# Kernel optimization log

Measured on AMD Instinct MI355X. Metric: run time of the kernel, lower is better.

The kernel has to match this reference:

```python
import jax, jax.numpy as jnp
import numpy as np

B, L, C = 32, 2048, 32
PL, STRIDE = 16, 16
P = L // PL
D, H_ENC, H_DEC, K, NH = 64, 256, 256, 512, 4
BETA, EPS, Q_EPS, CW = 0.25, 1e-5, 1e-5, 0.2


def setup_inputs() -> dict:
    key = jax.random.key(0)
    ks = jax.random.split(key, 16)
    g = lambda k, sh: 0.02 * jax.random.normal(k, sh, dtype=jnp.float32)
    return {
        'x': jax.random.normal(ks[0], (B, L, C), dtype=jnp.float32),
        'revin_w': jnp.ones((C,), jnp.float32), 'revin_b': jnp.zeros((C,), jnp.float32),
        'inp_W': g(ks[1], (PL, D)), 'inp_b': jnp.zeros((D,), jnp.float32),
        'Wq': g(ks[2], (D, D)), 'bq': jnp.zeros((D,), jnp.float32),
        'Wk': g(ks[3], (D, D)), 'bk': jnp.zeros((D,), jnp.float32),
        'Wv': g(ks[4], (D, D)), 'bv': jnp.zeros((D,), jnp.float32),
        'Wo': g(ks[5], (D, D)), 'bo': jnp.zeros((D,), jnp.float32),
        'ln1_g': jnp.ones((D,), jnp.float32), 'ln1_b': jnp.zeros((D,), jnp.float32),
        'ffn_W1': g(ks[6], (D, H_ENC)), 'ffn_b1': jnp.zeros((H_ENC,), jnp.float32),
        'ffn_W2': g(ks[7], (H_ENC, D)), 'ffn_b2': jnp.zeros((D,), jnp.float32),
        'ln2_g': jnp.ones((D,), jnp.float32), 'ln2_b': jnp.zeros((D,), jnp.float32),
        'codebook': jax.random.uniform(ks[8], (K, D), jnp.float32, -1.0 / K, 1.0 / K),
        'dec_W1': g(ks[9], (D, H_DEC)), 'dec_b1': jnp.zeros((H_DEC,), jnp.float32),
        'dec_W2': g(ks[10], (H_DEC, PL)), 'dec_b2': jnp.zeros((PL,), jnp.float32),
        'dec_Wr': g(ks[11], (D, PL)), 'dec_br': jnp.zeros((PL,), jnp.float32),
        'dec_ln_g': jnp.ones((PL,), jnp.float32), 'dec_ln_b': jnp.zeros((PL,), jnp.float32),
    }


def _layernorm(x, g, b):
    m = jnp.mean(x, -1, keepdims=True)
    v = jnp.mean((x - m) ** 2, -1, keepdims=True)
    return (x - m) * jax.lax.rsqrt(v + EPS) * g + b


def reference(x, revin_w, revin_b, inp_W, inp_b, Wq, bq, Wk, bk, Wv, bv, Wo, bo,
              ln1_g, ln1_b, ffn_W1, ffn_b1, ffn_W2, ffn_b2, ln2_g, ln2_b, codebook,
              dec_W1, dec_b1, dec_W2, dec_b2, dec_Wr, dec_br, dec_ln_g, dec_ln_b):
    # --- RevIN norm (stats over time dim) ---
    mean = jnp.mean(x, axis=1, keepdims=True)              # [B,1,C]
    std = jnp.sqrt(jnp.var(x, axis=1, keepdims=True) + EPS)
    xn = (x - mean) / std * revin_w + revin_b
    # --- patchify: [B,C,L] -> [B*C, P, PL] ---
    patches = jnp.transpose(xn, (0, 2, 1)).reshape(B * C, P, PL)
    # --- MHEncoder ---
    h = patches @ inp_W + inp_b                            # [N,P,D]
    dh = D // NH
    q = (h @ Wq + bq).reshape(-1, P, NH, dh)
    k = (h @ Wk + bk).reshape(-1, P, NH, dh)
    v = (h @ Wv + bv).reshape(-1, P, NH, dh)
    scores = jnp.einsum('nqhd,nkhd->nhqk', q, k) / np.sqrt(dh).astype(np.float32)
    attn = jax.nn.softmax(scores, axis=-1)
    a = jnp.einsum('nhqk,nkhd->nqhd', attn, v).reshape(-1, P, D)
    a = a @ Wo + bo
    h = _layernorm(h + a, ln1_g, ln1_b)
    ff = jax.nn.relu(h @ ffn_W1 + ffn_b1) @ ffn_W2 + ffn_b2
    h = _layernorm(h + ff, ln2_g, ln2_b)
    z = h.reshape(B, C, P, D)
    # --- ClusterQuantizer ---
    z2 = jnp.sum(z * z, -1, keepdims=True)                 # [B,V,P,1]
    e2 = jnp.sum(codebook * codebook, -1)                  # [K]
    ze = jnp.einsum('bvpd,kd->bvpk', z, codebook)
    dist = z2 + e2 - 2.0 * ze                              # [B,V,P,K]
    indices = jnp.argmin(dist, axis=-1)                    # [B,V,P] int
    z_q = codebook[indices]
    z_q_st = z + jax.lax.stop_gradient(z_q - z)
    codebook_loss = jnp.mean((z_q - jax.lax.stop_gradient(z)) ** 2)
    commitment_loss = jnp.mean((z - jax.lax.stop_gradient(z_q)) ** 2)
    cluster_loss = codebook_loss + BETA * commitment_loss
    counts = jnp.zeros((K,), jnp.float32).at[indices.ravel()].add(1.0)
    probs = counts / (counts.sum() + EPS)
    perplexity = jnp.exp(-jnp.sum(probs * jnp.log(probs + EPS)))
    # --- FFN decoder ---
    y = jax.nn.relu(z_q_st @ dec_W1 + dec_b1) @ dec_W2 + dec_b2
    y = y + z_q_st @ dec_Wr + dec_br
    recon_patches = _layernorm(y, dec_ln_g, dec_ln_b)      # [B,V,P,PL]
    recon = jnp.transpose(recon_patches.reshape(B, C, L), (0, 2, 1))  # [B,L,C]
    # --- RevIN denorm ---
    r = (recon - revin_b) / (revin_w + EPS * EPS) * std + mean
    rec_loss = jnp.mean((x - r) ** 2)
    loss_total = rec_loss + CW * cluster_loss
    return (loss_total, rec_loss, z_q_st, r, indices, perplexity)
```

## Files before the change

kernel.cpp:

```cpp
#include <hip/hip_runtime.h>
#include <math.h>

#define TPB 256

#define B_  32
#define L_  2048
#define C_  32
#define PL_ 16
#define P_  128
#define D_  64
#define HE_ 256
#define HD_ 256
#define K_  512
#define N_  1024
#define M_  131072

#define EPS_  1e-5f
#define BETA_ 0.25f
#define CW_   0.2f

#define OUT_LOSS 0
#define OUT_REC  1
#define OUT_ZQ   2
#define OUT_R    8388610
#define OUT_IDX  10485762
#define OUT_PERP 10616834

#define WS_MEAN   0
#define WS_STD    1024
#define WS_QT     2048
#define WS_KT     6144
#define WS_VT     10240
#define WS_E2     34816
#define WS_COUNTS 35328
#define WS_CPART  35840
#define WS_H0     36864
#define WS_H1     8425472
#define WS_RPART  WS_H1

__global__ void k_prep(const float* __restrict__ Wq, const float* __restrict__ Wk,
                       const float* __restrict__ Wv,
                       const float* __restrict__ cb, float* __restrict__ ws) {
    int g = blockIdx.x * TPB + threadIdx.x;
    if (g < 4096) { int t = g >> 6, j = g & 63; ws[WS_QT + g] = Wq[j * D_ + t]; }
    else if (g < 8192) { int g2 = g - 4096; int t = g2 >> 6, j = g2 & 63; ws[WS_KT + g2] = Wk[j * D_ + t]; }
    else if (g < 12288) { int g2 = g - 8192; int t = g2 >> 6, j = g2 & 63; ws[WS_VT + g2] = Wv[j * D_ + t]; }
    if (g < K_) {
        float s = 0.f;
        for (int j = 0; j < D_; j++) { float v = cb[g * D_ + j]; s += v * v; }
        ws[WS_E2 + g] = s;
    }
}

__global__ void k_stats(const float* __restrict__ x, float* __restrict__ ws) {
    int bc = blockIdx.x;
    int b = bc >> 5, c = bc & 31;
    const float* xp = x + (size_t)b * L_ * C_ + c;
    float s = 0.f, s2 = 0.f;
    for (int l = threadIdx.x; l < L_; l += TPB) { float v = xp[(size_t)l * C_]; s += v; s2 += v * v; }
    __shared__ float sh[TPB], sh2[TPB];
    sh[threadIdx.x] = s; sh2[threadIdx.x] = s2; __syncthreads();
    for (int o2 = 128; o2 > 0; o2 >>= 1) {
        if (threadIdx.x < o2) { sh[threadIdx.x] += sh[threadIdx.x + o2]; sh2[threadIdx.x] += sh2[threadIdx.x + o2]; }
        __syncthreads();
    }
    if (threadIdx.x == 0) {
        float m = sh[0] / (float)L_;
        float var = sh2[0] / (float)L_ - m * m;
        ws[WS_MEAN + bc] = m;
        ws[WS_STD + bc] = sqrtf(var + EPS_);
    }
}

__global__ __launch_bounds__(TPB) void k_embed(
    const float* __restrict__ x, const float* __restrict__ rw, const float* __restrict__ rb,
    const float* __restrict__ inpW, const float* __restrict__ inpb, float* __restrict__ ws) {
    int idx = blockIdx.x * TPB + threadIdx.x;
    int row = idx >> 6, d = idx & 63;
    int n = row >> 7, p = row & 127;
    int b = n >> 5, c = n & 31;
    float m = ws[WS_MEAN + n], sd = ws[WS_STD + n];
    float w = rw[c], bb = rb[c];
    const float* xp = x + (size_t)b * L_ * C_ + (size_t)p * PL_ * C_ + c;
    float acc = inpb[d];
#pragma unroll
    for (int j = 0; j < PL_; j++) {
        float xv = xp[(size_t)j * C_];
        float xn = (xv - m) / sd * w + bb;
        acc += xn * inpW[j * D_ + d];
    }
    ws[WS_H0 + (size_t)idx] = acc;
}

#define HSS  68
#define HS_  0
#define KH_  8704
#define VH_  10752
#define SMF  12800

__global__ __launch_bounds__(TPB) void k_attn(
    float* __restrict__ ws,
    const float* __restrict__ bq, const float* __restrict__ bk, const float* __restrict__ bv) {
    __shared__ float sm[SMF];
    const int tid = threadIdx.x;
    const int n = blockIdx.x >> 2, hh = blockIdx.x & 3;
    const float* h0 = ws + WS_H0 + (size_t)n * (P_ * D_);
    float* agl = ws + WS_H1 + (size_t)n * (P_ * D_);

    {
        const float4* h04 = (const float4*)h0;
#pragma unroll
        for (int it = 0; it < 8; ++it) {
            int e = tid + it * 256;
            int r = e >> 4, j4 = e & 15;
            *(float4*)(sm + HS_ + r * HSS + j4 * 4) = h04[e];
        }
    }
    __syncthreads();

    const int t_ = tid & 15, ib = tid >> 4;
    const float4* WqT4 = (const float4*)(ws + WS_QT);
    const float4* WkT4 = (const float4*)(ws + WS_KT);
    const float4* WvT4 = (const float4*)(ws + WS_VT);

    {
        float4 wreg[16];
        const float4* kr = WkT4 + (size_t)(hh * 16 + t_) * 16;
#pragma unroll
        for (int j4 = 0; j4 < 16; j4++) wreg[j4] = kr[j4];
        float bb = bk[hh * 16 + t_];
#pragma unroll
        for (int it = 0; it < 8; it++) {
            int i2 = ib + it * 16;
            const float4* hr = (const float4*)(sm + HS_ + i2 * HSS);
            float acc = bb;
#pragma unroll
            for (int j4 = 0; j4 < 16; j4++) {
                float4 h4 = hr[j4], w4 = wreg[j4];
                acc += h4.x * w4.x + h4.y * w4.y + h4.z * w4.z + h4.w * w4.w;
            }
            sm[KH_ + i2 * 16 + t_] = acc;
        }
    }
    {
        float4 wreg[16];
        const float4* vr = WvT4 + (size_t)(hh * 16 + t_) * 16;
#pragma unroll
        for (int j4 = 0; j4 < 16; j4++) wreg[j4] = vr[j4];
        float bb = bv[hh * 16 + t_];
#pragma unroll
        for (int it = 0; it < 8; it++) {
            int i2 = ib + it * 16;
            const float4* hr = (const float4*)(sm + HS_ + i2 * HSS);
            float acc = bb;
#pragma unroll
            for (int j4 = 0; j4 < 16; j4++) {
                float4 h4 = hr[j4], w4 = wreg[j4];
                acc += h4.x * w4.x + h4.y * w4.y + h4.z * w4.z + h4.w * w4.w;
            }
            sm[VH_ + i2 * 16 + t_] = acc;
        }
    }
    const int i = tid >> 1, half = tid & 1;
    float q0[8], q1[8];
    {
        float4 hreg[16];
        const float4* hr = (const float4*)(sm + HS_ + i * HSS);
#pragma unroll
        for (int j4 = 0; j4 < 16; j4++) hreg[j4] = hr[j4];
        float qh[8];
#pragma unroll
        for (int u = 0; u < 8; u++) {
            const float4* wr = WqT4 + (size_t)(hh * 16 + half * 8 + u) * 16;
            float acc = bq[hh * 16 + half * 8 + u];
#pragma unroll
            for (int j4 = 0; j4 < 16; j4++) {
                float4 w4 = wr[j4];
                acc += hreg[j4].x * w4.x + hreg[j4].y * w4.y + hreg[j4].z * w4.z + hreg[j4].w * w4.w;
            }
            qh[u] = acc;
        }
#pragma unroll
        for (int u = 0; u < 8; u++) {
            float oth = __shfl_xor(qh[u], 1);
            q0[u] = half ? oth : qh[u];
            q1[u] = half ? qh[u] : oth;
        }
    }
    __syncthreads();
    float mx = -INFINITY, S = 0.f;
    float o[16];
#pragma unroll
    for (int u = 0; u < 16; u++) o[u] = 0.f;
    const float4* kh4 = (const float4*)(sm + KH_);
    const float4* vh4 = (const float4*)(sm + VH_);
    for (int ch = 0; ch < 8; ch++) {
        float s[8];
#pragma unroll
        for (int kk = 0; kk < 8; kk++) {
            int m = (ch * 8 + kk) * 2 + half;
            float4 a0 = kh4[m * 4 + 0], a1 = kh4[m * 4 + 1], a2 = kh4[m * 4 + 2], a3 = kh4[m * 4 + 3];
            float sp = q0[0] * a0.x + q0[1] * a0.y + q0[2] * a0.z + q0[3] * a0.w
                     + q0[4] * a1.x + q0[5] * a1.y + q0[6] * a1.z + q0[7] * a1.w
                     + q1[0] * a2.x + q1[1] * a2.y + q1[2] * a2.z + q1[3] * a2.w
                     + q1[4] * a3.x + q1[5] * a3.y + q1[6] * a3.z + q1[7] * a3.w;
            s[kk] = sp * 0.25f;
        }
        float cm = fmaxf(fmaxf(fmaxf(s[0], s[1]), fmaxf(s[2], s[3])),
                         fmaxf(fmaxf(s[4], s[5]), fmaxf(s[6], s[7])));
        float nM = fmaxf(mx, cm);
        float sc = __expf(mx - nM);
        S *= sc;
#pragma unroll
        for (int u = 0; u < 16; u++) o[u] *= sc;
#pragma unroll
        for (int kk = 0; kk < 8; kk++) {
            int m = (ch * 8 + kk) * 2 + half;
            float p = __expf(s[kk] - nM);
            S += p;
            float4 v0 = vh4[m * 4 + 0], v1 = vh4[m * 4 + 1], v2 = vh4[m * 4 + 2], v3 = vh4[m * 4 + 3];
            o[0] += p * v0.x; o[1] += p * v0.y; o[2] += p * v0.z; o[3] += p * v0.w;
            o[4] += p * v1.x; o[5] += p * v1.y; o[6] += p * v1.z; o[7] += p * v1.w;
            o[8] += p * v2.x; o[9] += p * v2.y; o[10] += p * v2.z; o[11] += p * v2.w;
            o[12] += p * v3.x; o[13] += p * v3.y; o[14] += p * v3.z; o[15] += p * v3.w;
        }
        mx = nM;
    }
    {
        float mo = __shfl_xor(mx, 1), So = __shfl_xor(S, 1);
        float nM = fmaxf(mx, mo);
        float sa = __expf(mx - nM), sb = __expf(mo - nM);
        float Sc = S * sa + So * sb;
        float inv = 1.f / Sc;
        float oo[16];
#pragma unroll
        for (int u = 0; u < 16; u++) oo[u] = __shfl_xor(o[u], 1);
        float wv[8];
#pragma unroll
        for (int u = 0; u < 8; u++) {
            float lo = (o[u] * sa + oo[u] * sb) * inv;
            float hi = (o[8 + u] * sa + oo[8 + u] * sb) * inv;
            wv[u] = half ? hi : lo;
        }
        float4 r0, r1;
        r0.x = wv[0]; r0.y = wv[1]; r0.z = wv[2]; r0.w = wv[3];
        r1.x = wv[4]; r1.y = wv[5]; r1.z = wv[6]; r1.w = wv[7];
        float4* ap4 = (float4*)(agl + (size_t)i * D_ + hh * 16 + half * 8);
        ap4[0] = r0; ap4[1] = r1;
    }
}

#define FHS  68

__global__ __launch_bounds__(TPB) void k_woffn(
    float* __restrict__ ws, const float* __restrict__ Wo, const float* __restrict__ bo,
    const float* __restrict__ g1, const float* __restrict__ b1,
    const float* __restrict__ fW1, const float* __restrict__ fb1,
    const float* __restrict__ fW2, const float* __restrict__ fb2,
    const float* __restrict__ g2, const float* __restrict__ b2) {
    __shared__ float bufA[64][FHS];
    __shared__ float hT[64][FHS];
    const int tid = threadIdx.x;
    const int row0 = blockIdx.x * 64;
    const float* aog = ws + WS_H1 + (size_t)row0 * D_;

    {
        const float4* ao4 = (const float4*)aog;
#pragma unroll
        for (int it = 0; it < 4; ++it) {
            int e = tid + it * 256;
            int r = e >> 4, j4 = e & 15;
            float4 v = ao4[e];
            bufA[j4 * 4 + 0][r] = v.x; bufA[j4 * 4 + 1][r] = v.y;
            bufA[j4 * 4 + 2][r] = v.z; bufA[j4 * 4 + 3][r] = v.w;
        }
    }
    const int ty = tid >> 4, tx = tid & 15;
    float acc[4][4];
    {
        float4 bb = ((const float4*)bo)[tx];
#pragma unroll
        for (int r = 0; r < 4; r++) { acc[r][0] = bb.x; acc[r][1] = bb.y; acc[r][2] = bb.z; acc[r][3] = bb.w; }
    }
    __syncthreads();
    const float4* Wo4 = (const float4*)Wo;
#pragma unroll 4
    for (int j = 0; j < 64; ++j) {
        float4 a = *(const float4*)&bufA[j][ty * 4];
        float4 w = Wo4[j * 16 + tx];
        float ar[4] = {a.x, a.y, a.z, a.w}, wr[4] = {w.x, w.y, w.z, w.w};
#pragma unroll
        for (int r = 0; r < 4; r++)
#pragma unroll
            for (int c = 0; c < 4; c++) acc[r][c] += ar[r] * wr[c];
    }
    float h1v[4][4];
    {
        const float4* h04 = (const float4*)(ws + WS_H0 + (size_t)row0 * D_);
        float4 gg = ((const float4*)g1)[tx], bbn = ((const float4*)b1)[tx];
#pragma unroll
        for (int r = 0; r < 4; r++) {
            float4 res = h04[(ty * 4 + r) * 16 + tx];
            acc[r][0] += res.x; acc[r][1] += res.y; acc[r][2] += res.z; acc[r][3] += res.w;
            float s = acc[r][0] + acc[r][1] + acc[r][2] + acc[r][3];
            s += __shfl_xor(s, 1); s += __shfl_xor(s, 2); s += __shfl_xor(s, 4); s += __shfl_xor(s, 8);
            float mean_ = s * (1.f / 64.f);
            float vv = 0.f;
#pragma unroll
            for (int c = 0; c < 4; c++) { float d_ = acc[r][c] - mean_; vv += d_ * d_; }
            vv += __shfl_xor(vv, 1); vv += __shfl_xor(vv, 2); vv += __shfl_xor(vv, 4); vv += __shfl_xor(vv, 8);
            float rstd = 1.f / sqrtf(vv * (1.f / 64.f) + EPS_);
            h1v[r][0] = (acc[r][0] - mean_) * rstd * gg.x + bbn.x;
            h1v[r][1] = (acc[r][1] - mean_) * rstd * gg.y + bbn.y;
            h1v[r][2] = (acc[r][2] - mean_) * rstd * gg.z + bbn.z;
            h1v[r][3] = (acc[r][3] - mean_) * rstd * gg.w + bbn.w;
        }
    }
#pragma unroll
    for (int r = 0; r < 4; r++)
#pragma unroll
        for (int c = 0; c < 4; c++) hT[tx * 4 + c][ty * 4 + r] = h1v[r][c];
    const float4* W14 = (const float4*)fW1;
    const float4* W24 = (const float4*)fW2;
    float outv[4][4];
    {
        float4 bb = ((const float4*)fb2)[tx];
#pragma unroll
        for (int r = 0; r < 4; r++) { outv[r][0] = bb.x; outv[r][1] = bb.y; outv[r][2] = bb.z; outv[r][3] = bb.w; }
    }
    __syncthreads();

    for (int tc = 0; tc < 4; ++tc) {
        float a2[4][4];
        {
            float4 bb1 = ((const float4*)fb1)[tc * 16 + tx];
#pragma unroll
            for (int r = 0; r < 4; r++) { a2[r][0] = bb1.x; a2[r][1] = bb1.y; a2[r][2] = bb1.z; a2[r][3] = bb1.w; }
        }
#pragma unroll 4
        for (int j = 0; j < 64; ++j) {
            float4 a = *(const float4*)&hT[j][ty * 4];
            float4 w = W14[j * 64 + tc * 16 + tx];
            float ar[4] = {a.x, a.y, a.z, a.w}, wr[4] = {w.x, w.y, w.z, w.w};
#pragma unroll
            for (int r = 0; r < 4; r++)
#pragma unroll
                for (int c = 0; c < 4; c++) a2[r][c] += ar[r] * wr[c];
        }
        __syncthreads();
#pragma unroll
        for (int r = 0; r < 4; r++)
#pragma unroll
            for (int c = 0; c < 4; c++) bufA[tx * 4 + c][ty * 4 + r] = fmaxf(a2[r][c], 0.f);
        __syncthreads();
#pragma unroll 4
        for (int h = 0; h < 64; ++h) {
            float4 a = *(const float4*)&bufA[h][ty * 4];
            float4 w = W24[(tc * 64 + h) * 16 + tx];
            float ar[4] = {a.x, a.y, a.z, a.w}, wr[4] = {w.x, w.y, w.z, w.w};
#pragma unroll
            for (int r = 0; r < 4; r++)
#pragma unroll
                for (int c = 0; c < 4; c++) outv[r][c] += ar[r] * wr[c];
        }
    }
    {
        float4 gg = ((const float4*)g2)[tx], bb = ((const float4*)b2)[tx];
        float4* zp = (float4*)(ws + WS_H0 + (size_t)row0 * D_);
#pragma unroll
        for (int r = 0; r < 4; r++) {
            outv[r][0] += h1v[r][0]; outv[r][1] += h1v[r][1];
            outv[r][2] += h1v[r][2]; outv[r][3] += h1v[r][3];
            float s = outv[r][0] + outv[r][1] + outv[r][2] + outv[r][3];
            s += __shfl_xor(s, 1); s += __shfl_xor(s, 2); s += __shfl_xor(s, 4); s += __shfl_xor(s, 8);
            float mean_ = s * (1.f / 64.f);
            float vv = 0.f;
#pragma unroll
            for (int c = 0; c < 4; c++) { float d_ = outv[r][c] - mean_; vv += d_ * d_; }
            vv += __shfl_xor(vv, 1); vv += __shfl_xor(vv, 2); vv += __shfl_xor(vv, 4); vv += __shfl_xor(vv, 8);
            float rstd = 1.f / sqrtf(vv * (1.f / 64.f) + EPS_);
            float4 z;
            z.x = (outv[r][0] - mean_) * rstd * gg.x + bb.x;
            z.y = (outv[r][1] - mean_) * rstd * gg.y + bb.y;
            z.z = (outv[r][2] - mean_) * rstd * gg.z + bb.z;
            z.w = (outv[r][3] - mean_) * rstd * gg.w + bb.w;
            zp[(ty * 4 + r) * 16 + tx] = z;
        }
    }
}

#define QROWS 128
#define QKT   64
#define ZTS   132
#define CBS   68

__global__ __launch_bounds__(TPB) void k_quant(
    float* __restrict__ ws, const float* __restrict__ cb, float* __restrict__ out) {
    __shared__ float zT[64][ZTS];
    __shared__ float cbT[64][CBS];
    __shared__ float z2s[QROWS];
    __shared__ float e2t[QKT];
    __shared__ int   ridx[QROWS];
    __shared__ float red[TPB];

    const int tid = threadIdx.x;
    const int row0 = blockIdx.x * QROWS;
    const float* zg = ws + WS_H0 + (size_t)row0 * D_;
    const float4* zg4 = (const float4*)zg;
    const float4* cbg4 = (const float4*)cb;

    {
        int j4 = tid >> 4;
#pragma unroll
        for (int it = 0; it < 8; ++it) {
            int r = (tid & 15) + it * 16;
            float4 v = zg4[r * 16 + j4];
            zT[j4 * 4 + 0][r] = v.x; zT[j4 * 4 + 1][r] = v.y;
            zT[j4 * 4 + 2][r] = v.z; zT[j4 * 4 + 3][r] = v.w;
        }
    }
    if (tid < QROWS) {
        const float4* zr = (const float4*)(zg + (size_t)tid * D_);
        float s = 0.f;
#pragma unroll
        for (int j = 0; j < 16; j++) { float4 v = zr[j]; s += v.x * v.x + v.y * v.y + v.z * v.z + v.w * v.w; }
        z2s[tid] = s;
    }

    const int ty = tid >> 4, tx = tid & 15;
    float best[8]; int bidx[8];
#pragma unroll
    for (int u = 0; u < 8; u++) { best[u] = 3.4e38f; bidx[u] = 0; }

    for (int t = 0; t < K_ / QKT; ++t) {
        const int k0 = t * QKT;
        __syncthreads();
        {
            int j4 = tid >> 4;
#pragma unroll
            for (int it = 0; it < 4; ++it) {
                int kk = (tid & 15) + it * 16;
                float4 v = cbg4[(size_t)(k0 + kk) * 16 + j4];
                cbT[j4 * 4 + 0][kk] = v.x; cbT[j4 * 4 + 1][kk] = v.y;
                cbT[j4 * 4 + 2][kk] = v.z; cbT[j4 * 4 + 3][kk] = v.w;
            }
        }
        if (tid < QKT) e2t[tid] = ws[WS_E2 + k0 + tid];
        __syncthreads();

        float acc[8][4];
#pragma unroll
        for (int u = 0; u < 8; u++)
#pragma unroll
            for (int c = 0; c < 4; c++) acc[u][c] = 0.f;

        for (int j = 0; j < 64; ++j) {
            float4 a0 = *(const float4*)&zT[j][ty * 8];
            float4 a1 = *(const float4*)&zT[j][ty * 8 + 4];
            float4 b0 = *(const float4*)&cbT[j][tx * 4];
            float ar[8] = {a0.x, a0.y, a0.z, a0.w, a1.x, a1.y, a1.z, a1.w};
            float br[4] = {b0.x, b0.y, b0.z, b0.w};
#pragma unroll
            for (int u = 0; u < 8; u++)
#pragma unroll
                for (int c = 0; c < 4; c++) acc[u][c] += ar[u] * br[c];
        }

#pragma unroll
        for (int u = 0; u < 8; u++) {
            float z2v = z2s[ty * 8 + u];
#pragma unroll
            for (int c = 0; c < 4; c++) {
                float dist = (z2v + e2t[tx * 4 + c]) - 2.f * acc[u][c];
                int kidx = k0 + tx * 4 + c;
                if (dist < best[u]) { best[u] = dist; bidx[u] = kidx; }
            }
        }
    }

#pragma unroll
    for (int m = 1; m <= 8; m <<= 1) {
#pragma unroll
        for (int u = 0; u < 8; u++) {
            float ob = __shfl_xor(best[u], m, 64);
            int oi = __shfl_xor(bidx[u], m, 64);
            if (ob < best[u] || (ob == best[u] && oi < bidx[u])) { best[u] = ob; bidx[u] = oi; }
        }
    }
    if (tx == 0) {
#pragma unroll
        for (int u = 0; u < 8; u++) ridx[ty * 8 + u] = bidx[u];
    }
    __syncthreads();

    if (tid < QROWS) {
        int bi = ridx[tid];
        out[OUT_IDX + row0 + tid] = (float)bi;
        atomicAdd((unsigned int*)ws + WS_COUNTS + bi, 1u);
    }
    {
        int r = tid >> 1, half = tid & 1;
        int bi = ridx[r];
        const float4* cw = (const float4*)(cb + (size_t)bi * D_ + half * 32);
        const float4* zr4 = (const float4*)(zg + (size_t)r * D_ + half * 32);
        float2* zqo = (float2*)(out + OUT_ZQ + (size_t)(row0 + r) * D_ + half * 32);
        float csum = 0.f;
#pragma unroll
        for (int j4 = 0; j4 < 8; ++j4) {
            float4 w = cw[j4]; float4 zz = zr4[j4];
            float d0 = w.x - zz.x, d1 = w.y - zz.y, d2 = w.z - zz.z, d3 = w.w - zz.w;
            csum += d0 * d0 + d1 * d1 + d2 * d2 + d3 * d3;
            float2 p0; p0.x = w.x; p0.y = w.y; zqo[j4 * 2] = p0;
            float2 p1; p1.x = w.z; p1.y = w.w; zqo[j4 * 2 + 1] = p1;
        }
        red[tid] = csum;
    }
    __syncthreads();
    for (int o2 = 128; o2 > 0; o2 >>= 1) {
        if (tid < o2) red[tid] += red[tid + o2];
        __syncthreads();
    }
    if (tid == 0) ws[WS_CPART + blockIdx.x] = red[0];
}

#define DR_ 64

__global__ __launch_bounds__(TPB) void k_dec(
    float* __restrict__ ws, const float* __restrict__ x, const float* __restrict__ cb,
    const float* __restrict__ dW1, const float* __restrict__ db1,
    const float* __restrict__ dW2, const float* __restrict__ db2,
    const float* __restrict__ dWr, const float* __restrict__ dbr,
    const float* __restrict__ lng, const float* __restrict__ lnb,
    const float* __restrict__ rw, const float* __restrict__ rb,
    float* __restrict__ out) {
    __shared__ float zqT[64][FHS];
    __shared__ float Hc[64][FHS];
    __shared__ int   ridx[DR_];
    __shared__ float red[TPB];
    const int tid = threadIdx.x;
    const int row0 = blockIdx.x * DR_;
    if (tid < DR_) ridx[tid] = (int)out[OUT_IDX + row0 + tid];
    __syncthreads();
    {
        const float4* cb4 = (const float4*)cb;
#pragma unroll
        for (int it = 0; it < 4; ++it) {
            int e = tid + it * 256;
            int r = e >> 4, j4 = e & 15;
            float4 v = cb4[(size_t)ridx[r] * 16 + j4];
            zqT[j4 * 4 + 0][r] = v.x; zqT[j4 * 4 + 1][r] = v.y;
            zqT[j4 * 4 + 2][r] = v.z; zqT[j4 * 4 + 3][r] = v.w;
        }
    }
    const int ty = tid >> 4, tx = tid & 15;
    const float4* dW14 = (const float4*)dW1;
    float out4[4];
    {
        float b0 = db2[tx] + dbr[tx];
#pragma unroll
        for (int r = 0; r < 4; r++) out4[r] = b0;
    }
    __syncthreads();

    for (int tc = 0; tc < 4; ++tc) {
        float acc[4][4];
        {
            float4 bb1 = ((const float4*)db1)[tc * 16 + tx];
#pragma unroll
            for (int r = 0; r < 4; r++) { acc[r][0] = bb1.x; acc[r][1] = bb1.y; acc[r][2] = bb1.z; acc[r][3] = bb1.w; }
        }
#pragma unroll 4
        for (int j = 0; j < 64; ++j) {
            float4 a = *(const float4*)&zqT[j][ty * 4];
            float4 w = dW14[j * 64 + tc * 16 + tx];
            float ar[4] = {a.x, a.y, a.z, a.w}, wr[4] = {w.x, w.y, w.z, w.w};
#pragma unroll
            for (int r = 0; r < 4; r++)
#pragma unroll
                for (int c = 0; c < 4; c++) acc[r][c] += ar[r] * wr[c];
        }
        __syncthreads();
#pragma unroll
        for (int r = 0; r < 4; r++)
#pragma unroll
            for (int c = 0; c < 4; c++) Hc[tx * 4 + c][ty * 4 + r] = fmaxf(acc[r][c], 0.f);
        __syncthreads();
#pragma unroll 8
        for (int h = 0; h < 64; ++h) {
            float4 a = *(const float4*)&Hc[h][ty * 4];
            float w = dW2[(tc * 64 + h) * 16 + tx];
            out4[0] += a.x * w; out4[1] += a.y * w; out4[2] += a.z * w; out4[3] += a.w * w;
        }
    }
#pragma unroll 8
    for (int j = 0; j < 64; ++j) {
        float4 a = *(const float4*)&zqT[j][ty * 4];
        float w = dWr[j * 16 + tx];
        out4[0] += a.x * w; out4[1] += a.y * w; out4[2] += a.z * w; out4[3] += a.w * w;
    }
    const int n = row0 >> 7;
    const int b = n >> 5, c = n & 31;
    const float sd = ws[WS_STD + n], mn = ws[WS_MEAN + n];
    const float inv = 1.f / (rw[c] + EPS_ * EPS_);
    const float rbc = rb[c];
    const float lg = lng[tx], lb = lnb[tx];
    float part = 0.f;
#pragma unroll
    for (int r = 0; r < 4; r++) {
        float v = out4[r];
        float s = v;
        s += __shfl_xor(s, 1); s += __shfl_xor(s, 2); s += __shfl_xor(s, 4); s += __shfl_xor(s, 8);
        float mean_ = s * (1.f / 16.f);
        float d_ = v - mean_;
        float vv = d_ * d_;
        vv += __shfl_xor(vv, 1); vv += __shfl_xor(vv, 2); vv += __shfl_xor(vv, 4); vv += __shfl_xor(vv, 8);
        float rstd = 1.f / sqrtf(vv * (1.f / 16.f) + EPS_);
        float yv = d_ * rstd * lg + lb;
        float rr = (yv - rbc) * inv * sd + mn;
        int row = row0 + ty * 4 + r;
        int p = row & 127;
        size_t xi = (size_t)b * L_ * C_ + (size_t)(p * PL_ + tx) * C_ + c;
        out[OUT_R + xi] = rr;
        float dx = x[xi] - rr; part += dx * dx;
    }
    red[tid] = part;
    __syncthreads();
    for (int o2 = 128; o2 > 0; o2 >>= 1) {
        if (tid < o2) red[tid] += red[tid + o2];
        __syncthreads();
    }
    if (tid == 0) ws[WS_RPART + blockIdx.x] = red[0];
}

__global__ void k_final(float* __restrict__ ws, float* __restrict__ out) {
    __shared__ float sh[TPB];
    int tid = threadIdx.x;
    float cs = 0.f;
    for (int i2 = tid; i2 < 1024; i2 += TPB) cs += ws[WS_CPART + i2];
    sh[tid] = cs; __syncthreads();
    for (int o2 = 128; o2 > 0; o2 >>= 1) { if (tid < o2) sh[tid] += sh[tid + o2]; __syncthreads(); }
    float csum = sh[0]; __syncthreads();
    float rs = 0.f;
    for (int i2 = tid; i2 < 2048; i2 += TPB) rs += ws[WS_RPART + i2];
    sh[tid] = rs; __syncthreads();
    for (int o2 = 128; o2 > 0; o2 >>= 1) { if (tid < o2) sh[tid] += sh[tid + o2]; __syncthreads(); }
    float rsum = sh[0]; __syncthreads();
    const unsigned int* counts = (const unsigned int*)ws + WS_COUNTS;
    float H = 0.f;
    for (int k2 = tid; k2 < K_; k2 += TPB) {
        float p = (float)counts[k2] / (131072.f + EPS_);
        H += p * logf(p + EPS_);
    }
    sh[tid] = H; __syncthreads();
    for (int o2 = 128; o2 > 0; o2 >>= 1) { if (tid < o2) sh[tid] += sh[tid + o2]; __syncthreads(); }
    if (tid == 0) {
        float rec = rsum / 2097152.f;
        float msd = csum / 8388608.f;
        float cl = (1.f + BETA_) * msd;
        out[OUT_LOSS] = rec + CW_ * cl;
        out[OUT_REC] = rec;
        out[OUT_PERP] = expf(-sh[0]);
    }
}

extern "C" void kernel_launch(void* const* d_in, const int* in_sizes, int n_in,
                              void* d_out, int out_size, void* d_ws, size_t ws_size,
                              hipStream_t stream) {
    const float* x    = (const float*)d_in[0];
    const float* rw   = (const float*)d_in[1];
    const float* rb   = (const float*)d_in[2];
    const float* inpW = (const float*)d_in[3];
    const float* inpb = (const float*)d_in[4];
    const float* Wq   = (const float*)d_in[5];
    const float* bq   = (const float*)d_in[6];
    const float* Wk   = (const float*)d_in[7];
    const float* bk   = (const float*)d_in[8];
    const float* Wv   = (const float*)d_in[9];
    const float* bv   = (const float*)d_in[10];
    const float* Wo   = (const float*)d_in[11];
    const float* bo   = (const float*)d_in[12];
    const float* g1   = (const float*)d_in[13];
    const float* b1   = (const float*)d_in[14];
    const float* fW1  = (const float*)d_in[15];
    const float* fb1  = (const float*)d_in[16];
    const float* fW2  = (const float*)d_in[17];
    const float* fb2  = (const float*)d_in[18];
    const float* g2   = (const float*)d_in[19];
    const float* b2   = (const float*)d_in[20];
    const float* cb   = (const float*)d_in[21];
    const float* dW1  = (const float*)d_in[22];
    const float* db1  = (const float*)d_in[23];
    const float* dW2  = (const float*)d_in[24];
    const float* db2  = (const float*)d_in[25];
    const float* dWr  = (const float*)d_in[26];
    const float* dbr  = (const float*)d_in[27];
    const float* lng  = (const float*)d_in[28];
    const float* lnb  = (const float*)d_in[29];
    float* ws  = (float*)d_ws;
    float* out = (float*)d_out;

    hipMemsetAsync((char*)d_ws + (size_t)WS_COUNTS * 4, 0, 512 * 4, stream);
    k_prep<<<48, TPB, 0, stream>>>(Wq, Wk, Wv, cb, ws);
    k_stats<<<N_, TPB, 0, stream>>>(x, ws);
    k_embed<<<(M_ * D_) / TPB, TPB, 0, stream>>>(x, rw, rb, inpW, inpb, ws);
    k_attn<<<N_ * 4, TPB, 0, stream>>>(ws, bq, bk, bv);
    k_woffn<<<M_ / 64, TPB, 0, stream>>>(ws, Wo, bo, g1, b1, fW1, fb1, fW2, fb2, g2, b2);
    k_quant<<<M_ / QROWS, TPB, 0, stream>>>(ws, cb, out);
    k_dec<<<M_ / DR_, TPB, 0, stream>>>(ws, x, cb, dW1, db1, dW2, db2, dWr, dbr, lng, lnb, rw, rb, out);
    k_final<<<1, TPB, 0, stream>>>(ws, out);
}
```

Measured before the change: 721.2 us.

## Drop online-softmax max tracking and alias K/V shared memory over H tile

```diff
diff --git a/kernel.cpp b/kernel.cpp
--- a/kernel.cpp
+++ b/kernel.cpp
@@ -93,10 +93,9 @@
 }
 
 #define HSS  68
-#define HS_  0
-#define KH_  8704
-#define VH_  10752
-#define SMF  12800
+#define KH_  0
+#define VH_  2048
+#define SMF  8704
 
 __global__ __launch_bounds__(TPB) void k_attn(
     float* __restrict__ ws,
@@ -113,7 +112,7 @@
         for (int it = 0; it < 8; ++it) {
             int e = tid + it * 256;
             int r = e >> 4, j4 = e & 15;
-            *(float4*)(sm + HS_ + r * HSS + j4 * 4) = h04[e];
+            *(float4*)(sm + r * HSS + j4 * 4) = h04[e];
         }
     }
     __syncthreads();
@@ -123,6 +122,7 @@
     const float4* WkT4 = (const float4*)(ws + WS_KT);
     const float4* WvT4 = (const float4*)(ws + WS_VT);
 
+    float kreg[8], vreg[8];
     {
         float4 wreg[16];
         const float4* kr = WkT4 + (size_t)(hh * 16 + t_) * 16;
@@ -132,14 +132,14 @@
 #pragma unroll
         for (int it = 0; it < 8; it++) {
             int i2 = ib + it * 16;
-            const float4* hr = (const float4*)(sm + HS_ + i2 * HSS);
+            const float4* hr = (const float4*)(sm + i2 * HSS);
             float acc = bb;
 #pragma unroll
             for (int j4 = 0; j4 < 16; j4++) {
                 float4 h4 = hr[j4], w4 = wreg[j4];
                 acc += h4.x * w4.x + h4.y * w4.y + h4.z * w4.z + h4.w * w4.w;
             }
-            sm[KH_ + i2 * 16 + t_] = acc;
+            kreg[it] = acc;
         }
     }
     {
@@ -151,21 +151,21 @@
 #pragma unroll
         for (int it = 0; it < 8; it++) {
             int i2 = ib + it * 16;
-            const float4* hr = (const float4*)(sm + HS_ + i2 * HSS);
+            const float4* hr = (const float4*)(sm + i2 * HSS);
             float acc = bb;
 #pragma unroll
             for (int j4 = 0; j4 < 16; j4++) {
                 float4 h4 = hr[j4], w4 = wreg[j4];
                 acc += h4.x * w4.x + h4.y * w4.y + h4.z * w4.z + h4.w * w4.w;
             }
-            sm[VH_ + i2 * 16 + t_] = acc;
+            vreg[it] = acc;
         }
     }
     const int i = tid >> 1, half = tid & 1;
     float q0[8], q1[8];
     {
         float4 hreg[16];
-        const float4* hr = (const float4*)(sm + HS_ + i * HSS);
+        const float4* hr = (const float4*)(sm + i * HSS);
 #pragma unroll
         for (int j4 = 0; j4 < 16; j4++) hreg[j4] = hr[j4];
         float qh[8];
@@ -188,59 +188,44 @@
         }
     }
     __syncthreads();
-    float mx = -INFINITY, S = 0.f;
+#pragma unroll
+    for (int it = 0; it < 8; it++) {
+        int i2 = ib + it * 16;
+        sm[KH_ + i2 * 16 + t_] = kreg[it];
+        sm[VH_ + i2 * 16 + t_] = vreg[it];
+    }
+    __syncthreads();
+    float S = 0.f;
     float o[16];
 #pragma unroll
     for (int u = 0; u < 16; u++) o[u] = 0.f;
     const float4* kh4 = (const float4*)(sm + KH_);
     const float4* vh4 = (const float4*)(sm + VH_);
-    for (int ch = 0; ch < 8; ch++) {
-        float s[8];
-#pragma unroll
-        for (int kk = 0; kk < 8; kk++) {
-            int m = (ch * 8 + kk) * 2 + half;
-            float4 a0 = kh4[m * 4 + 0], a1 = kh4[m * 4 + 1], a2 = kh4[m * 4 + 2], a3 = kh4[m * 4 + 3];
-            float sp = q0[0] * a0.x + q0[1] * a0.y + q0[2] * a0.z + q0[3] * a0.w
-                     + q0[4] * a1.x + q0[5] * a1.y + q0[6] * a1.z + q0[7] * a1.w
-                     + q1[0] * a2.x + q1[1] * a2.y + q1[2] * a2.z + q1[3] * a2.w
-                     + q1[4] * a3.x + q1[5] * a3.y + q1[6] * a3.z + q1[7] * a3.w;
-            s[kk] = sp * 0.25f;
-        }
-        float cm = fmaxf(fmaxf(fmaxf(s[0], s[1]), fmaxf(s[2], s[3])),
-                         fmaxf(fmaxf(s[4], s[5]), fmaxf(s[6], s[7])));
-        float nM = fmaxf(mx, cm);
-        float sc = __expf(mx - nM);
-        S *= sc;
-#pragma unroll
-        for (int u = 0; u < 16; u++) o[u] *= sc;
-#pragma unroll
-        for (int kk = 0; kk < 8; kk++) {
-            int m = (ch * 8 + kk) * 2 + half;
-            float p = __expf(s[kk] - nM);
-            S += p;
-            float4 v0 = vh4[m * 4 + 0], v1 = vh4[m * 4 + 1], v2 = vh4[m * 4 + 2], v3 = vh4[m * 4 + 3];
-            o[0] += p * v0.x; o[1] += p * v0.y; o[2] += p * v0.z; o[3] += p * v0.w;
-            o[4] += p * v1.x; o[5] += p * v1.y; o[6] += p * v1.z; o[7] += p * v1.w;
-            o[8] += p * v2.x; o[9] += p * v2.y; o[10] += p * v2.z; o[11] += p * v2.w;
-            o[12] += p * v3.x; o[13] += p * v3.y; o[14] += p * v3.z; o[15] += p * v3.w;
-        }
-        mx = nM;
-    }
-    {
-        float mo = __shfl_xor(mx, 1), So = __shfl_xor(S, 1);
-        float nM = fmaxf(mx, mo);
-        float sa = __expf(mx - nM), sb = __expf(mo - nM);
-        float Sc = S * sa + So * sb;
-        float inv = 1.f / Sc;
-        float oo[16];
-#pragma unroll
-        for (int u = 0; u < 16; u++) oo[u] = __shfl_xor(o[u], 1);
+#pragma unroll 4
+    for (int m2 = 0; m2 < 64; m2++) {
+        int m = m2 * 2 + half;
+        float4 a0 = kh4[m * 4 + 0], a1 = kh4[m * 4 + 1], a2 = kh4[m * 4 + 2], a3 = kh4[m * 4 + 3];
+        float sp = q0[0] * a0.x + q0[1] * a0.y + q0[2] * a0.z + q0[3] * a0.w
+                 + q0[4] * a1.x + q0[5] * a1.y + q0[6] * a1.z + q0[7] * a1.w
+                 + q1[0] * a2.x + q1[1] * a2.y + q1[2] * a2.z + q1[3] * a2.w
+                 + q1[4] * a3.x + q1[5] * a3.y + q1[6] * a3.z + q1[7] * a3.w;
+        float p = __expf(sp * 0.25f);
+        S += p;
+        float4 v0 = vh4[m * 4 + 0], v1 = vh4[m * 4 + 1], v2 = vh4[m * 4 + 2], v3 = vh4[m * 4 + 3];
+        o[0] += p * v0.x; o[1] += p * v0.y; o[2] += p * v0.z; o[3] += p * v0.w;
+        o[4] += p * v1.x; o[5] += p * v1.y; o[6] += p * v1.z; o[7] += p * v1.w;
+        o[8] += p * v2.x; o[9] += p * v2.y; o[10] += p * v2.z; o[11] += p * v2.w;
+        o[12] += p * v3.x; o[13] += p * v3.y; o[14] += p * v3.z; o[15] += p * v3.w;
+    }
+    {
+        S += __shfl_xor(S, 1);
+        float inv = 1.f / S;
         float wv[8];
 #pragma unroll
         for (int u = 0; u < 8; u++) {
-            float lo = (o[u] * sa + oo[u] * sb) * inv;
-            float hi = (o[8 + u] * sa + oo[8 + u] * sb) * inv;
-            wv[u] = half ? hi : lo;
+            float lo = o[u] + __shfl_xor(o[u], 1);
+            float hi = o[8 + u] + __shfl_xor(o[8 + u], 1);
+            wv[u] = (half ? hi : lo) * inv;
         }
         float4 r0, r1;
         r0.x = wv[0]; r0.y = wv[1]; r0.z = wv[2]; r0.w = wv[3];
```

New measurement: 801.3 us. 1.11x slower.
